# Kernel tuning notes

Measured on AMD Instinct MI355X. Metric: run time of the kernel, lower is better.

The kernel has to match this reference:

```python
import jax, jax.numpy as jnp
import numpy as np


def _lstm_cell(x, h, c, Wih, Whh, bih, bhh):
    # torch.nn.LSTMCell: gates ordered (input, forget, cell, output)
    g = x @ Wih.T + h @ Whh.T + bih + bhh
    i, f, gg, o = jnp.split(g, 4, axis=-1)
    c2 = jax.nn.sigmoid(f) * c + jax.nn.sigmoid(i) * jnp.tanh(gg)
    h2 = jax.nn.sigmoid(o) * jnp.tanh(c2)
    return h2, c2


def setup_inputs() -> dict:
    key = jax.random.key(0)
    T, B, S, D = 64, 16, 128, 512
    ks = jax.random.split(key, 10)
    sc = 0.04  # ~ 1/sqrt(D) init scale
    z2 = jnp.zeros((B, D), jnp.float32)
    return {
        "emb_utts": jax.random.normal(ks[0], (T, B, D), jnp.float32),
        "M": jax.random.normal(ks[1], (B, S, D), jnp.float32),
        "hr0": z2, "cr0": z2, "hw0": z2, "cw0": z2,
        "Wih_r": jax.random.normal(ks[2], (4 * D, D), jnp.float32) * sc,
        "Whh_r": jax.random.normal(ks[3], (4 * D, D), jnp.float32) * sc,
        "bih_r": jnp.zeros((4 * D,), jnp.float32),
        "bhh_r": jnp.zeros((4 * D,), jnp.float32),
        "Wih_w": jax.random.normal(ks[4], (4 * D, D), jnp.float32) * sc,
        "Whh_w": jax.random.normal(ks[5], (4 * D, D), jnp.float32) * sc,
        "bih_w": jnp.zeros((4 * D,), jnp.float32),
        "bhh_w": jnp.zeros((4 * D,), jnp.float32),
        "Wc": jax.random.normal(ks[6], (D, 2 * D), jnp.float32) * sc,
        "bc": jnp.zeros((D,), jnp.float32),
    }


def reference(emb_utts, M, hr0, cr0, hw0, cw0,
              Wih_r, Whh_r, bih_r, bhh_r,
              Wih_w, Whh_w, bih_w, bhh_w, Wc, bc):
    def step(carry, w):
        hr, cr, hw, cw, Mc = carry
        # read LSTM (dropout is identity in eval)
        hr, cr = _lstm_cell(w, hr, cr, Wih_r, Whh_r, bih_r, bhh_r)
        # attention over memory
        sim = jnp.einsum('bd,bsd->bs', hr, Mc)
        z = jax.nn.softmax(sim, axis=-1)
        m = jnp.einsum('bs,bsd->bd', z, Mc)
        # compose + write LSTM
        comp = jnp.concatenate([hr, m], axis=-1) @ Wc.T + bc
        hw, cw = _lstm_cell(comp, hw, cw, Wih_w, Whh_w, bih_w, bhh_w)
        # memory update, faithful to source: M_new = (1 - z) * (M + hw)
        erase = 1.0 - z[:, :, None]
        Mc = erase * (Mc + hw[:, None, :])
        return (hr, cr, hw, cw, Mc), hw

    (hr, cr, hw, cw, Mf), outputs = jax.lax.scan(
        step, (hr0, cr0, hw0, cw0, M), emb_utts)
    return outputs, hr, cr, hw, cw, Mf
```

## Files before the change

### kernel.cpp

```cpp
#include <hip/hip_runtime.h>
#include <math.h>

#define TT 64
#define BB 16
#define SS 128
#define DD 512
#define NBLK 256
#define NTH 256
#define BD (BB*DD)
#define OUT_HR   (TT*BD)
#define OUT_CR   (OUT_HR + BD)
#define OUT_HW   (OUT_CR + BD)
#define OUT_CW   (OUT_HW + BD)
#define OUT_MF   (OUT_CW + BD)
#define MAGIC 0x13579BDFu

#define SY_SLOT 256

#define HRR_OFF 0
#define HWR_OFF 532480
#define MR_OFF  1064960
#define SP_OFF  1589248
#define GE_OFF  1622016

#define OFF_WHR  0
#define OFF_WHW  4672
#define OFF_WFH  9344
#define OFF_WFM  14016
#define OFF_ABUF 18688
#define OFF_ML   28160
#define OFF_PRED 32256
#define OFF_GFB  36480
#define OFF_GFT  36608
#define OFF_ZL   36736
#define OFF_BFL  36992
#define OFF_SMW  37000
#define LDS_FLOATS 37008
#define LDS_BYTES  (LDS_FLOATS*4)
#define KH_W 292
#define KH_A 592

#define COLC(c) (((c) >> 1) * DD + dr0 + ((c) & 1))

__device__ __forceinline__ float sigf(float x) { return 1.f / (1.f + __expf(-x)); }

__device__ __forceinline__ void stg(float* p, float v) {
  __hip_atomic_store(p, v, __ATOMIC_RELAXED, __HIP_MEMORY_SCOPE_AGENT);
}
__device__ __forceinline__ float ldga(const float* p) {
  return __hip_atomic_load(p, __ATOMIC_RELAXED, __HIP_MEMORY_SCOPE_AGENT);
}

__device__ __forceinline__ void barrive(unsigned* sync, unsigned& ep) {
  __syncthreads();
  ++ep;
  if (threadIdx.x == 0) {
    asm volatile("s_waitcnt vmcnt(0)" ::: "memory");
    __hip_atomic_store(sync + SY_SLOT + blockIdx.x * 8, ep,
                       __ATOMIC_RELAXED, __HIP_MEMORY_SCOPE_AGENT);
  }
}
__device__ __forceinline__ void bwait(unsigned* sync, unsigned ep) {
  const unsigned* slot = sync + SY_SLOT + threadIdx.x * 8;
  while (__hip_atomic_load(slot, __ATOMIC_RELAXED, __HIP_MEMORY_SCOPE_AGENT) < ep) {
    __builtin_amdgcn_s_sleep(1);
  }
  __syncthreads();
}
__device__ __forceinline__ void lbar(unsigned* sync, unsigned& ep) {
  barrive(sync, ep);
  bwait(sync, ep);
}

__device__ __forceinline__ float dotf4(const float* __restrict__ a,
                                       const float* __restrict__ b, int n4) {
  const float4* a4 = (const float4*)a;
  const float4* b4 = (const float4*)b;
  float4 s = make_float4(0.f, 0.f, 0.f, 0.f);
#pragma unroll 8
  for (int k = 0; k < n4; ++k) {
    float4 x = a4[k], y = b4[k];
    s.x = fmaf(x.x, y.x, s.x); s.y = fmaf(x.y, y.y, s.y);
    s.z = fmaf(x.z, y.z, s.z); s.w = fmaf(x.w, y.w, s.w);
  }
  return (s.x + s.y) + (s.z + s.w);
}

__device__ __forceinline__ void dot_pass8(const float* __restrict__ A,
                                          const float* __restrict__ W,
                                          float* __restrict__ pout)
{
  float acc[8] = {0.f,0.f,0.f,0.f,0.f,0.f,0.f,0.f};
#pragma unroll
  for (int j = 0; j < 8; ++j) {
    float4 a4 = *(const float4*)(A + j*4);
#pragma unroll
    for (int c = 0; c < 8; ++c) {
      float4 w4 = *(const float4*)(W + c*36 + j*4);
      acc[c] = fmaf(a4.x, w4.x, acc[c]); acc[c] = fmaf(a4.y, w4.y, acc[c]);
      acc[c] = fmaf(a4.z, w4.z, acc[c]); acc[c] = fmaf(a4.w, w4.w, acc[c]);
    }
  }
  *(float4*)(pout)   = make_float4(acc[0],acc[1],acc[2],acc[3]);
  *(float4*)(pout+4) = make_float4(acc[4],acc[5],acc[6],acc[7]);
}

__device__ __forceinline__ void dot_pass8g(const float* __restrict__ ag,
                                           const float* __restrict__ Wb,
                                           int khq,
                                           float* __restrict__ pout)
{
  float acc[8] = {0.f,0.f,0.f,0.f,0.f,0.f,0.f,0.f};
#pragma unroll
  for (int jj = 0; jj < 2; ++jj) {
    const float* Wt = Wb + (khq*2 + jj)*KH_W;
#pragma unroll
    for (int j = 0; j < 8; ++j) {
      float4 a4 = *(const float4*)(ag + jj*32 + j*4);
#pragma unroll
      for (int c = 0; c < 8; ++c) {
        float4 w4 = *(const float4*)(Wt + c*36 + j*4);
        acc[c] = fmaf(a4.x, w4.x, acc[c]); acc[c] = fmaf(a4.y, w4.y, acc[c]);
        acc[c] = fmaf(a4.z, w4.z, acc[c]); acc[c] = fmaf(a4.w, w4.w, acc[c]);
      }
    }
  }
  *(float4*)(pout)   = make_float4(acc[0],acc[1],acc[2],acc[3]);
  *(float4*)(pout+4) = make_float4(acc[4],acc[5],acc[6],acc[7]);
}

__global__ void __launch_bounds__(NTH) memnet(
    const float* __restrict__ emb, const float* __restrict__ M_in,
    const float* __restrict__ hr0, const float* __restrict__ cr0,
    const float* __restrict__ hw0, const float* __restrict__ cw0,
    const float* __restrict__ Wih_r, const float* __restrict__ Whh_r,
    const float* __restrict__ bih_r, const float* __restrict__ bhh_r,
    const float* __restrict__ Wih_w, const float* __restrict__ Whh_w,
    const float* __restrict__ bih_w, const float* __restrict__ bhh_w,
    const float* __restrict__ Wc, const float* __restrict__ bc,
    float* __restrict__ out,
    unsigned* sync, float* __restrict__ wsf)
{
  extern __shared__ float L[];
  const int tid = threadIdx.x;
  const int bid = blockIdx.x;

  const int mb  = bid & 15;
  const int mdh = bid >> 4;
  const int dr0 = 2 * bid;

  float* hrr = wsf + HRR_OFF;
  float* hwr = wsf + HWR_OFF;
  float* mr  = wsf + MR_OFF;
  float* sp  = wsf + SP_OFF;
  float* gE  = wsf + GE_OFF + bid * (TT * 128);

  if (bid == 0) {
    __hip_atomic_store(sync + SY_SLOT + tid * 8, 0u,
                       __ATOMIC_RELAXED, __HIP_MEMORY_SCOPE_AGENT);
    __syncthreads();
    if (tid == 0) {
      asm volatile("s_waitcnt vmcnt(0)" ::: "memory");
      __hip_atomic_store(sync, MAGIC, __ATOMIC_RELAXED, __HIP_MEMORY_SCOPE_AGENT);
    }
  } else if (tid == 0) {
    while (__hip_atomic_load(sync, __ATOMIC_RELAXED, __HIP_MEMORY_SCOPE_AGENT) != MAGIC) {}
  }
  __syncthreads();
  unsigned ep = 0;

  float cr = 0.f, cw = 0.f;
  if (tid >= 128 && tid < 160) {
    const int t = tid - 128, b = t & 15, dl = t >> 4;
    cr = cr0[b * DD + dr0 + dl];
    cw = cw0[b * DD + dr0 + dl];
  }

  {
    float* wih = L + OFF_ABUF;
#pragma unroll
    for (int c = 0; c < 8; ++c)
      ((float2*)(wih + c * DD))[tid] = ((const float2*)(Wih_w + COLC(c) * DD))[tid];
  }
  __syncthreads();
  {
    const float* wih = L + OFF_ABUF;
    float4 acc[8];
#pragma unroll
    for (int c = 0; c < 8; ++c) acc[c] = make_float4(0.f,0.f,0.f,0.f);
    const int k0 = tid * 4;
    for (int cc = 0; cc < DD; ++cc) {
      float4 wc4 = *(const float4*)(Wc + cc * 1024 + k0);
#pragma unroll
      for (int c = 0; c < 8; ++c) {
        const float wv = wih[c * DD + cc];
        acc[c].x = fmaf(wv, wc4.x, acc[c].x); acc[c].y = fmaf(wv, wc4.y, acc[c].y);
        acc[c].z = fmaf(wv, wc4.z, acc[c].z); acc[c].w = fmaf(wv, wc4.w, acc[c].w);
      }
    }
    const int kk = k0 & 511, kh = kk >> 5, jf = kk & 31;
    float* Tb = L + ((k0 < 512) ? OFF_WFH : OFF_WFM);
#pragma unroll
    for (int c = 0; c < 8; ++c)
      *(float4*)(Tb + kh*KH_W + c*36 + jf) = acc[c];
    if (tid < 8) {
      float s = 0.f;
      for (int cc = 0; cc < DD; ++cc) s = fmaf(wih[tid * DD + cc], bc[cc], s);
      L[OFF_BFL + tid] = s + bih_w[COLC(tid)] + bhh_w[COLC(tid)];
    }
  }
  __syncthreads();
  {
    const int c = tid >> 5, r = tid & 31;
    const int kk = r * 16, kh = kk >> 5, jb = (r & 1) * 16;
#pragma unroll
    for (int set = 0; set < 2; ++set) {
      const float* Wsrc = set ? Whh_w : Whh_r;
      float* dst = L + (set ? OFF_WHW : OFF_WHR) + kh*KH_W + c*36 + jb;
      const float* src = Wsrc + COLC(c) * DD + kk;
#pragma unroll
      for (int u = 0; u < 4; ++u)
        *(float4*)(dst + u*4) = *(const float4*)(src + u*4);
    }
  }
  {
    const int d_l = tid >> 3, sq = tid & 7;
    const int d = mdh * 32 + d_l;
#pragma unroll 4
    for (int j = 0; j < 16; ++j) {
      const int s = sq * 16 + j;
      L[OFF_ML + d_l * 128 + s] = M_in[(mb * SS + s) * DD + d];
    }
  }
  {
    const int tH = tid >> 7, b = (tid >> 3) & 15, c = tid & 7;
    const int col = COLC(c);
    const float bias = bih_r[col] + bhh_r[col];
    const float* wrow = Wih_r + col * DD;
    for (int t = tH * 32; t < tH * 32 + 32; ++t) {
      gE[t * 128 + b * 8 + c] = dotf4(emb + (t * BB + b) * DD, wrow, DD / 4) + bias;
    }
  }
  __syncthreads();
  {
#pragma unroll
    for (int j = 0; j < 8; ++j) {
      const int idx = j * 256 + tid;
      const int b = idx >> 7, k4 = idx & 127;
      const int kh = k4 >> 3, jf = (k4 & 7) * 4;
      float4 v = ((const float4*)hr0)[idx];
      *(float4*)(L + OFF_ABUF + kh*KH_A + b*36 + jf) = v;
    }
  }
  __syncthreads();
  {
    const int kh = tid >> 4, b = tid & 15;
    dot_pass8(L + OFF_ABUF + kh*KH_A + b*36, L + OFF_WHR + kh*KH_W,
              L + OFF_PRED + kh*132 + b*8);
  }
  __syncthreads();
  if (tid < 128) {
    float s = 0.f;
#pragma unroll
    for (int k2 = 0; k2 < 16; ++k2) s += L[OFF_PRED + k2*132 + tid];
    L[OFF_GFT + tid] = s;
  }
  __syncthreads();
  if (tid >= 128 && tid < 160) {
    const int t = tid - 128, b = t & 15, dl = t >> 4;
    float g[4];
#pragma unroll
    for (int q = 0; q < 4; ++q) {
      const int bc = b * 8 + q * 2 + dl;
      g[q] = L[OFF_GFT + bc] + gE[0 * 128 + bc];
    }
    cr = sigf(g[1]) * cr + sigf(g[0]) * tanhf(g[2]);
    const float h2 = sigf(g[3]) * tanhf(cr);
    stg(hrr + 1 * BD + b * DD + dr0 + dl, h2);
  }
  lbar(sync, ep);
  {
    const float* src = hrr + 1 * BD;
#pragma unroll
    for (int j = 0; j < 8; ++j) {
      const int idx = j * 256 + tid;
      const int b = idx >> 7, k4 = idx & 127;
      const int kh = k4 >> 3, jf = (k4 & 7) * 4;
      float4 v = ((const float4*)src)[idx];
      *(float4*)(L + OFF_ABUF + kh*KH_A + b*36 + jf) = v;
    }
  }
  __syncthreads();

  for (int i = 0; i < TT; ++i) {
    const int ii = i + 1;
    float* zold = L + OFF_ZL + ((i & 1) ^ 1) * 128;
    float* znew = L + OFF_ZL + (i & 1) * 128;

    {
      const int d_l = tid >> 3, sq = tid & 7;
      const float* Mrow = L + OFF_ML + d_l * 128;
      const float hrv = L[OFF_ABUF + mdh*KH_A + mb*36 + d_l];
#pragma unroll
      for (int j = 0; j < 4; ++j) {
        const int s4 = sq * 16 + j * 4;
        float4 M4 = *(const float4*)(Mrow + s4);
        float4 s;
        s.x = hrv * M4.x; s.y = hrv * M4.y; s.z = hrv * M4.z; s.w = hrv * M4.w;
        *(float4*)(L + OFF_PRED + d_l*132 + s4) = s;
      }
    }
    __syncthreads();
    if (tid < SS) {
      float v = 0.f;
#pragma unroll
      for (int dl2 = 0; dl2 < 32; ++dl2) v += L[OFF_PRED + dl2*132 + tid];
      stg(sp + (mb * 16 + mdh) * SS + tid, v);
    }
    barrive(sync, ep);

    if (ii < TT) {
      {
        const int kh = tid >> 4, b = tid & 15;
        dot_pass8(L + OFF_ABUF + kh*KH_A + b*36, L + OFF_WHR + kh*KH_W,
                  L + OFF_PRED + kh*132 + b*8);
      }
      __syncthreads();
      if (tid < 128) {
        float s = 0.f;
#pragma unroll
        for (int k2 = 0; k2 < 16; ++k2) s += L[OFF_PRED + k2*132 + tid];
        L[OFF_GFT + tid] = s;
      }
      __syncthreads();
      if (tid >= 128 && tid < 160) {
        const int t = tid - 128, b = t & 15, dl = t >> 4;
        float g[4];
#pragma unroll
        for (int q = 0; q < 4; ++q) {
          const int bc = b * 8 + q * 2 + dl;
          g[q] = L[OFF_GFT + bc] + gE[ii * 128 + bc];
        }
        cr = sigf(g[1]) * cr + sigf(g[0]) * tanhf(g[2]);
        const float h2 = sigf(g[3]) * tanhf(cr);
        stg(hrr + (ii + 1) * BD + b * DD + dr0 + dl, h2);
        if (ii == TT - 1) {
          out[OUT_HR + b * DD + dr0 + dl] = h2;
          out[OUT_CR + b * DD + dr0 + dl] = cr;
        }
      }
    }
    bwait(sync, ep);

    float vsum = 0.f;
    if (tid < SS) {
#pragma unroll
      for (int j = 0; j < 16; ++j) vsum += ldga(sp + (mb * 16 + j) * SS + tid);
    } else if (i > 0) {
      const int t = tid - 128, k0 = t * 4;
      const float4 hw4 = *(const float4*)(hwr + i * BD + mb * DD + k0);
      const float4 a4  = *(const float4*)(L + OFF_ABUF + (k0 >> 5)*KH_A + mb*36 + (k0 & 31));
      float p = a4.x * hw4.x;
      p = fmaf(a4.y, hw4.y, p); p = fmaf(a4.z, hw4.z, p); p = fmaf(a4.w, hw4.w, p);
      for (int off = 32; off > 0; off >>= 1) p += __shfl_xor(p, off);
      if ((tid & 63) == 0) L[OFF_SMW + 6 + ((tid >> 6) & 1)] = p;
    }
    __syncthreads();
    if (tid < SS) {
      float v = vsum;
      if (i > 0) {
        const float hrdot = L[OFF_SMW + 6] + L[OFF_SMW + 7];
        v = (1.f - zold[tid]) * (v + hrdot);
      }
      float wm = v;
      for (int off = 32; off > 0; off >>= 1) wm = fmaxf(wm, __shfl_xor(wm, off));
      if ((tid & 63) == 0) L[OFF_SMW + (tid >> 6)] = wm;
      vsum = v;
    }
    __syncthreads();
    if (tid < SS) {
      const float gmax = fmaxf(L[OFF_SMW], L[OFF_SMW + 1]);
      const float e = __expf(vsum - gmax);
      float sm = e;
      for (int off = 32; off > 0; off >>= 1) sm += __shfl_xor(sm, off);
      if ((tid & 63) == 0) L[OFF_SMW + 2 + (tid >> 6)] = sm;
      vsum = e;
    }
    __syncthreads();
    if (tid < SS) znew[tid] = vsum / (L[OFF_SMW + 2] + L[OFF_SMW + 3]);
    __syncthreads();
    {
      const int d_l = tid >> 3, sq = tid & 7;
      float* Mrow = L + OFF_ML + d_l * 128;
      float mv = 0.f;
      if (i > 0) {
        const float hwv = hwr[i * BD + mb * DD + mdh * 32 + d_l];
#pragma unroll
        for (int j = 0; j < 4; ++j) {
          const int s4 = sq * 16 + j * 4;
          float4 M4  = *(float4*)(Mrow + s4);
          float4 zo4 = *(const float4*)(zold + s4);
          float4 zn4 = *(const float4*)(znew + s4);
          M4.x = (1.f - zo4.x) * (M4.x + hwv);
          M4.y = (1.f - zo4.y) * (M4.y + hwv);
          M4.z = (1.f - zo4.z) * (M4.z + hwv);
          M4.w = (1.f - zo4.w) * (M4.w + hwv);
          *(float4*)(Mrow + s4) = M4;
          mv = fmaf(zn4.x, M4.x, mv); mv = fmaf(zn4.y, M4.y, mv);
          mv = fmaf(zn4.z, M4.z, mv); mv = fmaf(zn4.w, M4.w, mv);
        }
      } else {
#pragma unroll
        for (int j = 0; j < 4; ++j) {
          const int s4 = sq * 16 + j * 4;
          float4 M4  = *(const float4*)(Mrow + s4);
          float4 zn4 = *(const float4*)(znew + s4);
          mv = fmaf(zn4.x, M4.x, mv); mv = fmaf(zn4.y, M4.y, mv);
          mv = fmaf(zn4.z, M4.z, mv); mv = fmaf(zn4.w, M4.w, mv);
        }
      }
      L[OFF_PRED + d_l * 8 + sq] = mv;
    }
    __syncthreads();
    if (tid < 32) {
      float mv = 0.f;
#pragma unroll
      for (int j = 0; j < 8; ++j) mv += L[OFF_PRED + tid * 8 + j];
      stg(mr + i * BD + mb * DD + mdh * 32 + tid, mv);
    }
    barrive(sync, ep);

    {
      const int kh = tid >> 4, b = tid & 15;
      dot_pass8(L + OFF_ABUF + kh*KH_A + b*36, L + OFF_WFH + kh*KH_W,
                L + OFF_PRED + 2112 + kh*132 + b*8);
    }
    __syncthreads();
    if (tid < 128) {
      float s = 0.f;
#pragma unroll
      for (int k2 = 0; k2 < 16; ++k2) s += L[OFF_PRED + 2112 + k2*132 + tid];
      L[OFF_GFB + tid] = s;
    }
    bwait(sync, ep);

    {
      const int src = tid >> 7, khq = (tid >> 4) & 7, b = tid & 15;
      const float* ag;
      const float* Wb;
      if (src == 0) { ag = mr + i * BD + b * DD + khq * 64; Wb = L + OFF_WFM; }
      else {
        const float* hwsrc = (i == 0) ? hw0 : (hwr + i * BD);
        ag = hwsrc + b * DD + khq * 64; Wb = L + OFF_WHW;
      }
      dot_pass8g(ag, Wb, khq, L + OFF_PRED + (src * 8 + khq) * 132 + b * 8);
    }
    __syncthreads();
    if (tid < 128) {
      float s = 0.f;
#pragma unroll
      for (int k2 = 0; k2 < 16; ++k2) s += L[OFF_PRED + k2*132 + tid];
      L[OFF_GFT + tid] = s;
    }
    __syncthreads();
    if (tid >= 128 && tid < 160) {
      const int t = tid - 128, b = t & 15, dl = t >> 4;
      float g[4];
#pragma unroll
      for (int q = 0; q < 4; ++q) {
        const int c = q * 2 + dl, bc = b * 8 + c;
        g[q] = L[OFF_GFB + bc] + L[OFF_GFT + bc] + L[OFF_BFL + c];
      }
      cw = sigf(g[1]) * cw + sigf(g[0]) * tanhf(g[2]);
      const float h2 = sigf(g[3]) * tanhf(cw);
      const int d = dr0 + dl;
      stg(hwr + (i + 1) * BD + b * DD + d, h2);
      out[i * BD + b * DD + d] = h2;
      if (i == TT - 1) {
        out[OUT_HW + b * DD + d] = h2;
        out[OUT_CW + b * DD + d] = cw;
      }
    }
    if (i < TT - 1) {
      const float* src = hrr + (i + 2) * BD;
#pragma unroll
      for (int j = 0; j < 8; ++j) {
        const int idx = j * 256 + tid;
        const int b = idx >> 7, k4 = idx & 127;
        const int kh = k4 >> 3, jf = (k4 & 7) * 4;
        float4 v = ((const float4*)src)[idx];
        *(float4*)(L + OFF_ABUF + kh*KH_A + b*36 + jf) = v;
      }
    }
    __syncthreads();
  }

  lbar(sync, ep);

  {
    const int d_l = tid >> 3, sq = tid & 7;
    const int d = mdh * 32 + d_l;
    const float hwv = hwr[TT * BD + mb * DD + d];
    const float* zfin = L + OFF_ZL + ((TT - 1) & 1) * 128;
#pragma unroll 4
    for (int j = 0; j < 16; ++j) {
      const int s = sq * 16 + j;
      const float nv = (1.f - zfin[s]) * (L[OFF_ML + d_l * 128 + s] + hwv);
      out[OUT_MF + (mb * SS + s) * DD + d] = nv;
    }
  }
}

extern "C" void kernel_launch(void* const* d_in, const int* in_sizes, int n_in,
                              void* d_out, int out_size, void* d_ws, size_t ws_size,
                              hipStream_t stream) {
  (void)in_sizes; (void)n_in; (void)out_size; (void)ws_size;
  const float* emb   = (const float*)d_in[0];
  const float* M_in  = (const float*)d_in[1];
  const float* hr0   = (const float*)d_in[2];
  const float* cr0   = (const float*)d_in[3];
  const float* hw0   = (const float*)d_in[4];
  const float* cw0   = (const float*)d_in[5];
  const float* Wih_r = (const float*)d_in[6];
  const float* Whh_r = (const float*)d_in[7];
  const float* bih_r = (const float*)d_in[8];
  const float* bhh_r = (const float*)d_in[9];
  const float* Wih_w = (const float*)d_in[10];
  const float* Whh_w = (const float*)d_in[11];
  const float* bih_w = (const float*)d_in[12];
  const float* bhh_w = (const float*)d_in[13];
  const float* Wc    = (const float*)d_in[14];
  const float* bc    = (const float*)d_in[15];
  float* out = (float*)d_out;

  char* wsb = (char*)d_ws;
  unsigned* sync = (unsigned*)wsb;
  float* wsf = (float*)(wsb + 16384);

  hipFuncSetAttribute((const void*)memnet,
                      hipFuncAttributeMaxDynamicSharedMemorySize, LDS_BYTES);

  hipLaunchKernelGGL(memnet, dim3(NBLK), dim3(NTH), LDS_BYTES, stream,
                     emb, M_in, hr0, cr0, hw0, cw0,
                     Wih_r, Whh_r, bih_r, bhh_r,
                     Wih_w, Whh_w, bih_w, bhh_w, Wc, bc,
                     out, sync, wsf);
}
```

Measured before the change: 1.463 ms.

## Use sharded atomic-counter grid barrier and restructure attention softmax/memory update

Replaces the per-block flag grid barrier with 8 sharded atomic counters polled by a single thread, and cuts the number of block-level syncs per step. The score dot product now reads strided (padded) M rows directly in place of a staging pass through LDS. The hr·hw correction term is precomputed as block partials in global memory, and the softmax is done by one wavefront while other threads apply the memory erase concurrently. The m reduction switches to shuffles. Risks are contention on the atomic counters and extra global traffic for the correction partials.

```diff
diff --git a/kernel.cpp b/kernel.cpp
--- a/kernel.cpp
+++ b/kernel.cpp
@@ -15,13 +15,14 @@
 #define OUT_MF   (OUT_CW + BD)
 #define MAGIC 0x13579BDFu
 
-#define SY_SLOT 256
+#define SY_GSH 256
 
 #define HRR_OFF 0
 #define HWR_OFF 532480
 #define MR_OFF  1064960
 #define SP_OFF  1589248
 #define GE_OFF  1622016
+#define KP_OFF  3719168
 
 #define OFF_WHR  0
 #define OFF_WHW  4672
@@ -29,16 +30,16 @@
 #define OFF_WFM  14016
 #define OFF_ABUF 18688
 #define OFF_ML   28160
-#define OFF_PRED 32256
-#define OFF_GFB  36480
-#define OFF_GFT  36608
-#define OFF_ZL   36736
-#define OFF_BFL  36992
-#define OFF_SMW  37000
-#define LDS_FLOATS 37008
+#define OFF_PRED 32384
+#define OFF_GFB  36608
+#define OFF_GFT  36736
+#define OFF_ZL   36864
+#define OFF_BFL  37120
+#define LDS_FLOATS 37128
 #define LDS_BYTES  (LDS_FLOATS*4)
 #define KH_W 292
 #define KH_A 592
+#define MLS 132
 
 #define COLC(c) (((c) >> 1) * DD + dr0 + ((c) & 1))
 
@@ -51,24 +52,32 @@
   return __hip_atomic_load(p, __ATOMIC_RELAXED, __HIP_MEMORY_SCOPE_AGENT);
 }
 
-__device__ __forceinline__ void barrive(unsigned* sync, unsigned& ep) {
-  __syncthreads();
-  ++ep;
+__device__ __forceinline__ void barrive(unsigned* sync, unsigned& ep, int shard) {
+  __syncthreads();
   if (threadIdx.x == 0) {
+    ++ep;
     asm volatile("s_waitcnt vmcnt(0)" ::: "memory");
-    __hip_atomic_store(sync + SY_SLOT + blockIdx.x * 8, ep,
-                       __ATOMIC_RELAXED, __HIP_MEMORY_SCOPE_AGENT);
+    __hip_atomic_fetch_add(sync + SY_GSH + shard * 64, 1u,
+                           __ATOMIC_RELAXED, __HIP_MEMORY_SCOPE_AGENT);
   }
 }
 __device__ __forceinline__ void bwait(unsigned* sync, unsigned ep) {
-  const unsigned* slot = sync + SY_SLOT + threadIdx.x * 8;
-  while (__hip_atomic_load(slot, __ATOMIC_RELAXED, __HIP_MEMORY_SCOPE_AGENT) < ep) {
-    __builtin_amdgcn_s_sleep(1);
-  }
-  __syncthreads();
-}
-__device__ __forceinline__ void lbar(unsigned* sync, unsigned& ep) {
-  barrive(sync, ep);
+  if (threadIdx.x == 0) {
+    const unsigned target = ep * (unsigned)NBLK;
+    for (;;) {
+      unsigned s = 0;
+#pragma unroll
+      for (int k = 0; k < 8; ++k)
+        s += __hip_atomic_load(sync + SY_GSH + k * 64,
+                               __ATOMIC_RELAXED, __HIP_MEMORY_SCOPE_AGENT);
+      if (s >= target) break;
+      __builtin_amdgcn_s_sleep(1);
+    }
+  }
+  __syncthreads();
+}
+__device__ __forceinline__ void lbar(unsigned* sync, unsigned& ep, int shard) {
+  barrive(sync, ep, shard);
   bwait(sync, ep);
 }
 
@@ -144,6 +153,7 @@
   extern __shared__ float L[];
   const int tid = threadIdx.x;
   const int bid = blockIdx.x;
+  const int gsh = bid & 7;
 
   const int mb  = bid & 15;
   const int mdh = bid >> 4;
@@ -154,12 +164,13 @@
   float* mr  = wsf + MR_OFF;
   float* sp  = wsf + SP_OFF;
   float* gE  = wsf + GE_OFF + bid * (TT * 128);
+  float* Kp  = wsf + KP_OFF;
 
   if (bid == 0) {
-    __hip_atomic_store(sync + SY_SLOT + tid * 8, 0u,
-                       __ATOMIC_RELAXED, __HIP_MEMORY_SCOPE_AGENT);
-    __syncthreads();
     if (tid == 0) {
+#pragma unroll
+      for (int k = 0; k < 8; ++k)
+        __hip_atomic_store(sync + SY_GSH + k * 64, 0u, __ATOMIC_RELAXED, __HIP_MEMORY_SCOPE_AGENT);
       asm volatile("s_waitcnt vmcnt(0)" ::: "memory");
       __hip_atomic_store(sync, MAGIC, __ATOMIC_RELAXED, __HIP_MEMORY_SCOPE_AGENT);
     }
@@ -169,7 +180,7 @@
   __syncthreads();
   unsigned ep = 0;
 
-  float cr = 0.f, cw = 0.f;
+  float cr = 0.f, cw = 0.f, hrn = 0.f;
   if (tid >= 128 && tid < 160) {
     const int t = tid - 128, b = t & 15, dl = t >> 4;
     cr = cr0[b * DD + dr0 + dl];
@@ -229,7 +240,7 @@
 #pragma unroll 4
     for (int j = 0; j < 16; ++j) {
       const int s = sq * 16 + j;
-      L[OFF_ML + d_l * 128 + s] = M_in[(mb * SS + s) * DD + d];
+      L[OFF_ML + d_l * MLS + s] = M_in[(mb * SS + s) * DD + d];
     }
   }
   {
@@ -278,7 +289,7 @@
     const float h2 = sigf(g[3]) * tanhf(cr);
     stg(hrr + 1 * BD + b * DD + dr0 + dl, h2);
   }
-  lbar(sync, ep);
+  lbar(sync, ep, gsh);
   {
     const float* src = hrr + 1 * BD;
 #pragma unroll
@@ -297,27 +308,15 @@
     float* zold = L + OFF_ZL + ((i & 1) ^ 1) * 128;
     float* znew = L + OFF_ZL + (i & 1) * 128;
 
-    {
-      const int d_l = tid >> 3, sq = tid & 7;
-      const float* Mrow = L + OFF_ML + d_l * 128;
-      const float hrv = L[OFF_ABUF + mdh*KH_A + mb*36 + d_l];
-#pragma unroll
-      for (int j = 0; j < 4; ++j) {
-        const int s4 = sq * 16 + j * 4;
-        float4 M4 = *(const float4*)(Mrow + s4);
-        float4 s;
-        s.x = hrv * M4.x; s.y = hrv * M4.y; s.z = hrv * M4.z; s.w = hrv * M4.w;
-        *(float4*)(L + OFF_PRED + d_l*132 + s4) = s;
-      }
-    }
-    __syncthreads();
     if (tid < SS) {
+      const float* hrp = L + OFF_ABUF + mdh*KH_A + mb*36;
+      const float* Mc  = L + OFF_ML + tid;
       float v = 0.f;
-#pragma unroll
-      for (int dl2 = 0; dl2 < 32; ++dl2) v += L[OFF_PRED + dl2*132 + tid];
+#pragma unroll 8
+      for (int d = 0; d < 32; ++d) v = fmaf(hrp[d], Mc[d * MLS], v);
       stg(sp + (mb * 16 + mdh) * SS + tid, v);
     }
-    barrive(sync, ep);
+    barrive(sync, ep, gsh);
 
     if (ii < TT) {
       {
@@ -343,6 +342,7 @@
         }
         cr = sigf(g[1]) * cr + sigf(g[0]) * tanhf(g[2]);
         const float h2 = sigf(g[3]) * tanhf(cr);
+        hrn = h2;
         stg(hrr + (ii + 1) * BD + b * DD + dr0 + dl, h2);
         if (ii == TT - 1) {
           out[OUT_HR + b * DD + dr0 + dl] = h2;
@@ -352,83 +352,68 @@
     }
     bwait(sync, ep);
 
-    float vsum = 0.f;
-    if (tid < SS) {
-#pragma unroll
-      for (int j = 0; j < 16; ++j) vsum += ldga(sp + (mb * 16 + j) * SS + tid);
-    } else if (i > 0) {
-      const int t = tid - 128, k0 = t * 4;
-      const float4 hw4 = *(const float4*)(hwr + i * BD + mb * DD + k0);
-      const float4 a4  = *(const float4*)(L + OFF_ABUF + (k0 >> 5)*KH_A + mb*36 + (k0 & 31));
-      float p = a4.x * hw4.x;
-      p = fmaf(a4.y, hw4.y, p); p = fmaf(a4.z, hw4.z, p); p = fmaf(a4.w, hw4.w, p);
-      for (int off = 32; off > 0; off >>= 1) p += __shfl_xor(p, off);
-      if ((tid & 63) == 0) L[OFF_SMW + 6 + ((tid >> 6) & 1)] = p;
-    }
-    __syncthreads();
-    if (tid < SS) {
-      float v = vsum;
+    if (tid < 64) {
+      float K = 0.f;
       if (i > 0) {
-        const float hrdot = L[OFF_SMW + 6] + L[OFF_SMW + 7];
-        v = (1.f - zold[tid]) * (v + hrdot);
-      }
-      float wm = v;
+        const float* kb = Kp + mb * 256 + tid * 4;
+        float kp = ldga(kb) + ldga(kb + 1) + ldga(kb + 2) + ldga(kb + 3);
+#pragma unroll
+        for (int off = 32; off > 0; off >>= 1) kp += __shfl_xor(kp, off);
+        K = kp;
+      }
+      float va = 0.f, vb = 0.f;
+#pragma unroll
+      for (int j = 0; j < 16; ++j) {
+        const float* row = sp + (mb * 16 + j) * SS;
+        va += ldga(row + tid);
+        vb += ldga(row + tid + 64);
+      }
+      if (i > 0) {
+        va = (1.f - zold[tid])      * (va + K);
+        vb = (1.f - zold[tid + 64]) * (vb + K);
+      }
+      float wm = fmaxf(va, vb);
+#pragma unroll
       for (int off = 32; off > 0; off >>= 1) wm = fmaxf(wm, __shfl_xor(wm, off));
-      if ((tid & 63) == 0) L[OFF_SMW + (tid >> 6)] = wm;
-      vsum = v;
-    }
-    __syncthreads();
-    if (tid < SS) {
-      const float gmax = fmaxf(L[OFF_SMW], L[OFF_SMW + 1]);
-      const float e = __expf(vsum - gmax);
-      float sm = e;
+      const float ea = __expf(va - wm), eb = __expf(vb - wm);
+      float sm = ea + eb;
+#pragma unroll
       for (int off = 32; off > 0; off >>= 1) sm += __shfl_xor(sm, off);
-      if ((tid & 63) == 0) L[OFF_SMW + 2 + (tid >> 6)] = sm;
-      vsum = e;
-    }
-    __syncthreads();
-    if (tid < SS) znew[tid] = vsum / (L[OFF_SMW + 2] + L[OFF_SMW + 3]);
+      znew[tid]      = ea / sm;
+      znew[tid + 64] = eb / sm;
+    } else if (tid < 192 && i > 0) {
+      const int t2 = tid - 64, d_l = t2 >> 2, q = t2 & 3;
+      const float hwv = hwr[i * BD + mb * DD + mdh * 32 + d_l];
+      float* Mrow = L + OFF_ML + d_l * MLS;
+#pragma unroll
+      for (int j = 0; j < 8; ++j) {
+        const int s4 = q * 32 + j * 4;
+        float4 M4 = *(float4*)(Mrow + s4);
+        float4 z4 = *(const float4*)(zold + s4);
+        M4.x = (1.f - z4.x) * (M4.x + hwv);
+        M4.y = (1.f - z4.y) * (M4.y + hwv);
+        M4.z = (1.f - z4.z) * (M4.z + hwv);
+        M4.w = (1.f - z4.w) * (M4.w + hwv);
+        *(float4*)(Mrow + s4) = M4;
+      }
+    }
     __syncthreads();
     {
       const int d_l = tid >> 3, sq = tid & 7;
-      float* Mrow = L + OFF_ML + d_l * 128;
+      const float* Mrow = L + OFF_ML + d_l * MLS;
       float mv = 0.f;
-      if (i > 0) {
-        const float hwv = hwr[i * BD + mb * DD + mdh * 32 + d_l];
-#pragma unroll
-        for (int j = 0; j < 4; ++j) {
-          const int s4 = sq * 16 + j * 4;
-          float4 M4  = *(float4*)(Mrow + s4);
-          float4 zo4 = *(const float4*)(zold + s4);
-          float4 zn4 = *(const float4*)(znew + s4);
-          M4.x = (1.f - zo4.x) * (M4.x + hwv);
-          M4.y = (1.f - zo4.y) * (M4.y + hwv);
-          M4.z = (1.f - zo4.z) * (M4.z + hwv);
-          M4.w = (1.f - zo4.w) * (M4.w + hwv);
-          *(float4*)(Mrow + s4) = M4;
-          mv = fmaf(zn4.x, M4.x, mv); mv = fmaf(zn4.y, M4.y, mv);
-          mv = fmaf(zn4.z, M4.z, mv); mv = fmaf(zn4.w, M4.w, mv);
-        }
-      } else {
-#pragma unroll
-        for (int j = 0; j < 4; ++j) {
-          const int s4 = sq * 16 + j * 4;
-          float4 M4  = *(const float4*)(Mrow + s4);
-          float4 zn4 = *(const float4*)(znew + s4);
-          mv = fmaf(zn4.x, M4.x, mv); mv = fmaf(zn4.y, M4.y, mv);
-          mv = fmaf(zn4.z, M4.z, mv); mv = fmaf(zn4.w, M4.w, mv);
-        }
-      }
-      L[OFF_PRED + d_l * 8 + sq] = mv;
-    }
-    __syncthreads();
-    if (tid < 32) {
-      float mv = 0.f;
-#pragma unroll
-      for (int j = 0; j < 8; ++j) mv += L[OFF_PRED + tid * 8 + j];
-      stg(mr + i * BD + mb * DD + mdh * 32 + tid, mv);
-    }
-    barrive(sync, ep);
+#pragma unroll
+      for (int j = 0; j < 4; ++j) {
+        const int s4 = sq * 16 + j * 4;
+        float4 z4 = *(const float4*)(znew + s4);
+        float4 M4 = *(const float4*)(Mrow + s4);
+        mv = fmaf(z4.x, M4.x, mv); mv = fmaf(z4.y, M4.y, mv);
+        mv = fmaf(z4.z, M4.z, mv); mv = fmaf(z4.w, M4.w, mv);
+      }
+      mv += __shfl_xor(mv, 4); mv += __shfl_xor(mv, 2); mv += __shfl_xor(mv, 1);
+      if (sq == 0) stg(mr + i * BD + mb * DD + mdh * 32 + d_l, mv);
+    }
+    barrive(sync, ep, gsh);
 
     {
       const int kh = tid >> 4, b = tid & 15;
@@ -480,6 +465,9 @@
         out[OUT_HW + b * DD + d] = h2;
         out[OUT_CW + b * DD + d] = cw;
       }
+      float kp = hrn * h2;
+      kp += __shfl_xor(kp, 16);
+      if (i < TT - 1 && t < 16) stg(Kp + b * 256 + bid, kp);
     }
     if (i < TT - 1) {
       const float* src = hrr + (i + 2) * BD;
@@ -495,7 +483,7 @@
     __syncthreads();
   }
 
-  lbar(sync, ep);
+  lbar(sync, ep, gsh);
 
   {
     const int d_l = tid >> 3, sq = tid & 7;
@@ -505,7 +493,7 @@
 #pragma unroll 4
     for (int j = 0; j < 16; ++j) {
       const int s = sq * 16 + j;
-      const float nv = (1.f - zfin[s]) * (L[OFF_ML + d_l * 128 + s] + hwv);
+      const float nv = (1.f - zfin[s]) * (L[OFF_ML + d_l * MLS + s] + hwv);
       out[OUT_MF + (mb * SS + s) * DD + d] = nv;
     }
   }
```

New measurement: 1.492 ms. No clear change (+1.9%).

## Shard grid barrier counters, overlap hw recurrent dot, shuffle-reduce memory read

Applied to the files above, without the earlier changes.

The per-block flag grid barrier, where every thread polled a slot, is replaced by 8 sharded atomic counters polled by a single thread, to cut barrier polling traffic. The recurrent Whh_w·hw dot product moves before the barrier wait so it overlaps with the other blocks' arrival. The next-step hr prefetch is issued earlier into registers. Small LDS reductions become direct FMA loops and wave shuffles, and the M tile row stride is padded to 132. The cost is more register pressure, extra LDS, and atomic contention on the shared counters.

```diff
diff --git a/kernel.cpp b/kernel.cpp
--- a/kernel.cpp
+++ b/kernel.cpp
@@ -15,7 +15,7 @@
 #define OUT_MF   (OUT_CW + BD)
 #define MAGIC 0x13579BDFu
 
-#define SY_SLOT 256
+#define SY_GSH 256
 
 #define HRR_OFF 0
 #define HWR_OFF 532480
@@ -29,16 +29,18 @@
 #define OFF_WFM  14016
 #define OFF_ABUF 18688
 #define OFF_ML   28160
-#define OFF_PRED 32256
-#define OFF_GFB  36480
-#define OFF_GFT  36608
-#define OFF_ZL   36736
-#define OFF_BFL  36992
-#define OFF_SMW  37000
-#define LDS_FLOATS 37008
+#define OFF_PRED 32384
+#define OFF_HWD  36608
+#define OFF_GFB  37664
+#define OFF_GFT  37792
+#define OFF_ZL   37920
+#define OFF_BFL  38176
+#define OFF_SMW  38184
+#define LDS_FLOATS 38192
 #define LDS_BYTES  (LDS_FLOATS*4)
 #define KH_W 292
 #define KH_A 592
+#define MLS 132
 
 #define COLC(c) (((c) >> 1) * DD + dr0 + ((c) & 1))
 
@@ -51,24 +53,32 @@
   return __hip_atomic_load(p, __ATOMIC_RELAXED, __HIP_MEMORY_SCOPE_AGENT);
 }
 
-__device__ __forceinline__ void barrive(unsigned* sync, unsigned& ep) {
-  __syncthreads();
-  ++ep;
+__device__ __forceinline__ void barrive(unsigned* sync, unsigned& ep, int shard) {
+  __syncthreads();
   if (threadIdx.x == 0) {
+    ++ep;
     asm volatile("s_waitcnt vmcnt(0)" ::: "memory");
-    __hip_atomic_store(sync + SY_SLOT + blockIdx.x * 8, ep,
-                       __ATOMIC_RELAXED, __HIP_MEMORY_SCOPE_AGENT);
+    __hip_atomic_fetch_add(sync + SY_GSH + shard * 64, 1u,
+                           __ATOMIC_RELAXED, __HIP_MEMORY_SCOPE_AGENT);
   }
 }
 __device__ __forceinline__ void bwait(unsigned* sync, unsigned ep) {
-  const unsigned* slot = sync + SY_SLOT + threadIdx.x * 8;
-  while (__hip_atomic_load(slot, __ATOMIC_RELAXED, __HIP_MEMORY_SCOPE_AGENT) < ep) {
-    __builtin_amdgcn_s_sleep(1);
-  }
-  __syncthreads();
-}
-__device__ __forceinline__ void lbar(unsigned* sync, unsigned& ep) {
-  barrive(sync, ep);
+  if (threadIdx.x == 0) {
+    const unsigned target = ep * (unsigned)NBLK;
+    for (;;) {
+      unsigned s = 0;
+#pragma unroll
+      for (int k = 0; k < 8; ++k)
+        s += __hip_atomic_load(sync + SY_GSH + k * 64,
+                               __ATOMIC_RELAXED, __HIP_MEMORY_SCOPE_AGENT);
+      if (s >= target) break;
+      __builtin_amdgcn_s_sleep(1);
+    }
+  }
+  __syncthreads();
+}
+__device__ __forceinline__ void lbar(unsigned* sync, unsigned& ep, int shard) {
+  barrive(sync, ep, shard);
   bwait(sync, ep);
 }
 
@@ -144,6 +154,7 @@
   extern __shared__ float L[];
   const int tid = threadIdx.x;
   const int bid = blockIdx.x;
+  const int gsh = bid & 7;
 
   const int mb  = bid & 15;
   const int mdh = bid >> 4;
@@ -156,10 +167,10 @@
   float* gE  = wsf + GE_OFF + bid * (TT * 128);
 
   if (bid == 0) {
-    __hip_atomic_store(sync + SY_SLOT + tid * 8, 0u,
-                       __ATOMIC_RELAXED, __HIP_MEMORY_SCOPE_AGENT);
-    __syncthreads();
     if (tid == 0) {
+#pragma unroll
+      for (int k = 0; k < 8; ++k)
+        __hip_atomic_store(sync + SY_GSH + k * 64, 0u, __ATOMIC_RELAXED, __HIP_MEMORY_SCOPE_AGENT);
       asm volatile("s_waitcnt vmcnt(0)" ::: "memory");
       __hip_atomic_store(sync, MAGIC, __ATOMIC_RELAXED, __HIP_MEMORY_SCOPE_AGENT);
     }
@@ -229,7 +240,7 @@
 #pragma unroll 4
     for (int j = 0; j < 16; ++j) {
       const int s = sq * 16 + j;
-      L[OFF_ML + d_l * 128 + s] = M_in[(mb * SS + s) * DD + d];
+      L[OFF_ML + d_l * MLS + s] = M_in[(mb * SS + s) * DD + d];
     }
   }
   {
@@ -278,7 +289,7 @@
     const float h2 = sigf(g[3]) * tanhf(cr);
     stg(hrr + 1 * BD + b * DD + dr0 + dl, h2);
   }
-  lbar(sync, ep);
+  lbar(sync, ep, gsh);
   {
     const float* src = hrr + 1 * BD;
 #pragma unroll
@@ -297,27 +308,15 @@
     float* zold = L + OFF_ZL + ((i & 1) ^ 1) * 128;
     float* znew = L + OFF_ZL + (i & 1) * 128;
 
-    {
-      const int d_l = tid >> 3, sq = tid & 7;
-      const float* Mrow = L + OFF_ML + d_l * 128;
-      const float hrv = L[OFF_ABUF + mdh*KH_A + mb*36 + d_l];
-#pragma unroll
-      for (int j = 0; j < 4; ++j) {
-        const int s4 = sq * 16 + j * 4;
-        float4 M4 = *(const float4*)(Mrow + s4);
-        float4 s;
-        s.x = hrv * M4.x; s.y = hrv * M4.y; s.z = hrv * M4.z; s.w = hrv * M4.w;
-        *(float4*)(L + OFF_PRED + d_l*132 + s4) = s;
-      }
-    }
-    __syncthreads();
     if (tid < SS) {
+      const float* hrp = L + OFF_ABUF + mdh*KH_A + mb*36;
+      const float* Mc  = L + OFF_ML + tid;
       float v = 0.f;
-#pragma unroll
-      for (int dl2 = 0; dl2 < 32; ++dl2) v += L[OFF_PRED + dl2*132 + tid];
+#pragma unroll 8
+      for (int d = 0; d < 32; ++d) v = fmaf(hrp[d], Mc[d * MLS], v);
       stg(sp + (mb * 16 + mdh) * SS + tid, v);
     }
-    barrive(sync, ep);
+    barrive(sync, ep, gsh);
 
     if (ii < TT) {
       {
@@ -391,7 +390,7 @@
     __syncthreads();
     {
       const int d_l = tid >> 3, sq = tid & 7;
-      float* Mrow = L + OFF_ML + d_l * 128;
+      float* Mrow = L + OFF_ML + d_l * MLS;
       float mv = 0.f;
       if (i > 0) {
         const float hwv = hwr[i * BD + mb * DD + mdh * 32 + d_l];
@@ -419,16 +418,10 @@
           mv = fmaf(zn4.z, M4.z, mv); mv = fmaf(zn4.w, M4.w, mv);
         }
       }
-      L[OFF_PRED + d_l * 8 + sq] = mv;
-    }
-    __syncthreads();
-    if (tid < 32) {
-      float mv = 0.f;
-#pragma unroll
-      for (int j = 0; j < 8; ++j) mv += L[OFF_PRED + tid * 8 + j];
-      stg(mr + i * BD + mb * DD + mdh * 32 + tid, mv);
-    }
-    barrive(sync, ep);
+      mv += __shfl_xor(mv, 4); mv += __shfl_xor(mv, 2); mv += __shfl_xor(mv, 1);
+      if (sq == 0) stg(mr + i * BD + mb * DD + mdh * 32 + d_l, mv);
+    }
+    barrive(sync, ep, gsh);
 
     {
       const int kh = tid >> 4, b = tid & 15;
@@ -441,25 +434,32 @@
 #pragma unroll
       for (int k2 = 0; k2 < 16; ++k2) s += L[OFF_PRED + 2112 + k2*132 + tid];
       L[OFF_GFB + tid] = s;
+    } else {
+      const int khq = (tid >> 4) & 7, b = tid & 15;
+      const float* hwsrc = (i == 0) ? hw0 : (hwr + i * BD);
+      dot_pass8g(hwsrc + b * DD + khq * 64, L + OFF_WHW, khq,
+                 L + OFF_HWD + khq * 132 + b * 8);
     }
     bwait(sync, ep);
 
+    float4 hrv[8];
+    if (i < TT - 1) {
+      const float* src = hrr + (i + 2) * BD;
+#pragma unroll
+      for (int j = 0; j < 8; ++j) hrv[j] = ((const float4*)src)[j * 256 + tid];
+    }
     {
-      const int src = tid >> 7, khq = (tid >> 4) & 7, b = tid & 15;
-      const float* ag;
-      const float* Wb;
-      if (src == 0) { ag = mr + i * BD + b * DD + khq * 64; Wb = L + OFF_WFM; }
-      else {
-        const float* hwsrc = (i == 0) ? hw0 : (hwr + i * BD);
-        ag = hwsrc + b * DD + khq * 64; Wb = L + OFF_WHW;
-      }
-      dot_pass8g(ag, Wb, khq, L + OFF_PRED + (src * 8 + khq) * 132 + b * 8);
+      const int khq = tid >> 4, b = tid & 15;
+      dot_pass8(mr + i * BD + b * DD + khq * 32, L + OFF_WFM + khq * KH_W,
+                L + OFF_PRED + khq * 132 + b * 8);
     }
     __syncthreads();
     if (tid < 128) {
       float s = 0.f;
 #pragma unroll
       for (int k2 = 0; k2 < 16; ++k2) s += L[OFF_PRED + k2*132 + tid];
+#pragma unroll
+      for (int k2 = 0; k2 < 8;  ++k2) s += L[OFF_HWD + k2*132 + tid];
       L[OFF_GFT + tid] = s;
     }
     __syncthreads();
@@ -482,20 +482,18 @@
       }
     }
     if (i < TT - 1) {
-      const float* src = hrr + (i + 2) * BD;
 #pragma unroll
       for (int j = 0; j < 8; ++j) {
         const int idx = j * 256 + tid;
         const int b = idx >> 7, k4 = idx & 127;
         const int kh = k4 >> 3, jf = (k4 & 7) * 4;
-        float4 v = ((const float4*)src)[idx];
-        *(float4*)(L + OFF_ABUF + kh*KH_A + b*36 + jf) = v;
-      }
-    }
-    __syncthreads();
-  }
-
-  lbar(sync, ep);
+        *(float4*)(L + OFF_ABUF + kh*KH_A + b*36 + jf) = hrv[j];
+      }
+    }
+    __syncthreads();
+  }
+
+  lbar(sync, ep, gsh);
 
   {
     const int d_l = tid >> 3, sq = tid & 7;
@@ -505,7 +503,7 @@
 #pragma unroll 4
     for (int j = 0; j < 16; ++j) {
       const int s = sq * 16 + j;
-      const float nv = (1.f - zfin[s]) * (L[OFF_ML + d_l * 128 + s] + hwv);
+      const float nv = (1.f - zfin[s]) * (L[OFF_ML + d_l * MLS + s] + hwv);
       out[OUT_MF + (mb * SS + s) * DD + d] = nv;
     }
   }
```

Measured after the change: 1.653 ms. 1.13x slower.
